# Optimization experiments

Hardware: AMD Instinct MI355X
Metric: run time of the kernel (lower is better)

## Reference

```python
import jax, jax.numpy as jnp
import numpy as np

N, E, D_IN, D_H = 20000, 320000, 512, 512
ALPHA = 0.1
LAMBDA = 1.0

def setup_inputs() -> dict:
    key = jax.random.key(0)
    ks = jax.random.split(key, 12)
    feat = jax.random.normal(ks[0], (N, D_IN), dtype=jnp.float32)
    src = jax.random.randint(ks[1], (E,), 0, N, dtype=jnp.int32)
    dst = jax.random.randint(ks[2], (E,), 0, N, dtype=jnp.int32)
    s = 0.05
    fc_w = jax.random.normal(ks[3], (D_H, D_IN), dtype=jnp.float32) * s  # torch Linear: [out,in]
    fc_b = jax.random.normal(ks[4], (D_H,), dtype=jnp.float32) * s
    w1_1 = jax.random.normal(ks[5], (D_H, D_H), dtype=jnp.float32) * s
    w2_1 = jax.random.normal(ks[6], (D_H, D_H), dtype=jnp.float32) * s
    b_1 = jax.random.normal(ks[7], (D_H,), dtype=jnp.float32) * s
    w1_2 = jax.random.normal(ks[8], (D_H, D_H), dtype=jnp.float32) * s
    w2_2 = jax.random.normal(ks[9], (D_H, D_H), dtype=jnp.float32) * s
    b_2 = jax.random.normal(ks[10], (D_H,), dtype=jnp.float32) * s
    return {"feat": feat, "src": src, "dst": dst, "fc_w": fc_w, "fc_b": fc_b,
            "w1_1": w1_1, "w2_1": w2_1, "b_1": b_1,
            "w1_2": w1_2, "w2_2": w2_2, "b_2": b_2}


def _gcn2_layer(h, h0, src, dst, norm, w1, w2, b, layer):
    # DGL GCN2Conv (project_initial_features=False)
    beta = float(np.log(LAMBDA / layer + 1.0))
    x = h * norm                      # [N, D]
    agg = jax.ops.segment_sum(x[src], dst, num_segments=h.shape[0])  # SpMM: sum over in-neighbors
    agg = agg * norm
    f = agg * (1.0 - ALPHA)
    f0 = h0 * ALPHA
    rst = ((1.0 - beta) * f + beta * (f @ w1)
           + (1.0 - beta) * f0 + beta * (f0 @ w2) + b)
    return jax.nn.relu(rst)


def reference(feat, src, dst, fc_w, fc_b, w1_1, w2_1, b_1, w1_2, w2_2, b_2):
    n = feat.shape[0]
    h = feat @ fc_w.T + fc_b          # initial projection
    # symmetric norm from in-degrees (clamped at 1), as in DGL
    deg = jax.ops.segment_sum(jnp.ones_like(dst, dtype=h.dtype), dst, num_segments=n)
    norm = jnp.clip(deg, 1.0, None) ** -0.5
    norm = norm[:, None]
    res = _gcn2_layer(h, h, src, dst, norm, w1_1, w2_1, b_1, layer=1)
    out = _gcn2_layer(res, h, src, dst, norm, w1_2, w2_2, b_2, layer=2)
    return out
```

## Files before the change

### kernel.cpp

```cpp
#include <hip/hip_runtime.h>
#include <hip/hip_bf16.h>
#include <stdint.h>
#include <stddef.h>

typedef __bf16 bf16_t;
typedef __bf16 bf16x4 __attribute__((ext_vector_type(4)));
typedef __bf16 bf16x8 __attribute__((ext_vector_type(8)));
typedef float floatx4 __attribute__((ext_vector_type(4)));

#define NN 20000
#define EE 320000
#define DD 512
#define CAP 96
#define BETA1 0.6931471805599453f
#define BETA2 0.40546510810816444f

__device__ __forceinline__ void gload16(const bf16_t* g, bf16_t* l) {
  __builtin_amdgcn_global_load_lds((const __attribute__((address_space(1))) uint32_t*)g,
                                   (__attribute__((address_space(3))) uint32_t*)l, 16, 0, 0);
}

__global__ __launch_bounds__(256) void bucket_kernel(
    const int* __restrict__ src, const int* __restrict__ dst,
    int* __restrict__ cnt, int* __restrict__ esrc, int E) {
  int e = blockIdx.x * 256 + threadIdx.x;
  if (e < E) {
    int d = dst[e];
    int pos = atomicAdd(&cnt[d], 1);
    if (pos < CAP) esrc[d * CAP + pos] = src[e];
  }
}

#define PREP_BLOCKS 7594
__global__ __launch_bounds__(256) void prep_kernel(
    const float* __restrict__ feat, const float* __restrict__ fc_w,
    const float* __restrict__ w1_1, const float* __restrict__ w2_1,
    const float* __restrict__ w1_2, const float* __restrict__ w2_2,
    bf16_t* __restrict__ featb, bf16_t* __restrict__ bw0,
    bf16_t* __restrict__ bt1, bf16_t* __restrict__ bt2,
    int* __restrict__ cnt, int* __restrict__ esrc) {
  int b = blockIdx.x, t = threadIdx.x;
  if (b < 5128) {
    const float* in = (b < 5000) ? feat : fc_w;
    bf16_t* out = (b < 5000) ? featb : bw0;
    size_t c = (size_t)(b < 5000 ? b : b - 5000) * 256 + t;
    const float* s = in + c * 8;
    float4 v0 = *(const float4*)s, v1 = *(const float4*)(s + 4);
    bf16x8 o = {(bf16_t)v0.x, (bf16_t)v0.y, (bf16_t)v0.z, (bf16_t)v0.w,
                (bf16_t)v1.x, (bf16_t)v1.y, (bf16_t)v1.z, (bf16_t)v1.w};
    *(bf16x8*)(out + c * 8) = o;
  } else if (b < 5640) {
    int base = (b < 5384) ? 5128 : 5384;
    const float* Wa = (b < 5384) ? w1_1 : w1_2;
    const float* Wb = (b < 5384) ? w2_1 : w2_2;
    bf16_t* bt = (b < 5384) ? bt1 : bt2;
    int c = (b - base) * 256 + t;
    int n = c >> 7, kc = c & 127;
    const float* W = (kc < 64) ? Wa : Wb;
    const float sc = (kc < 64) ? 1.0f : 0.1f;
    int kcw = kc & 63;
    bf16x8 o;
#pragma unroll
    for (int e = 0; e < 8; ++e)
      o[e] = (bf16_t)(sc * W[(size_t)(kcw * 8 + e) * 512 + n]);
    *(bf16x8*)(bt + (size_t)n * 1024 + kc * 8) = o;
  } else if (b < 5719) {
    int i = (b - 5640) * 256 + t;
    if (i < NN) cnt[i] = 0;
  } else {
    int i = (b - 5719) * 256 + t;
    ((int4*)esrc)[i] = make_int4(0, 0, 0, 0);
  }
}

__global__ __launch_bounds__(256) void aggregate_kernel(
    const bf16_t* __restrict__ hs, const int* __restrict__ cnt,
    const int* __restrict__ esrc, bf16_t* __restrict__ Acat) {
  __shared__ bf16_t ring[4][2][4][512];
  const int w = threadIdx.x >> 6;
  const int lane = threadIdx.x & 63;
  const int node = blockIdx.x * 4 + w;
  const int* eb = esrc + (size_t)node * CAP;
  int ncnt = cnt[node];
  int n_e = ncnt < CAP ? ncnt : CAP;
  float nd = 0.9f * rsqrtf(fmaxf((float)ncnt, 1.0f));
  int nchunks = (n_e + 3) >> 2;

  float acc[8] = {};
  bf16_t* r0base = &ring[w][0][0][lane * 8];
  bf16_t* r1base = &ring[w][1][0][lane * 8];

  int4 icur, inext;

  asm volatile("s_waitcnt vmcnt(0)" ::: "memory");
  __builtin_amdgcn_sched_barrier(0);
  icur = *(const int4*)(eb);
  asm volatile("s_waitcnt vmcnt(0)" ::: "memory");
  __builtin_amdgcn_sched_barrier(0);
  inext = *(const int4*)(eb + 4);
  gload16(hs + (size_t)icur.x * DD + lane * 8, r0base);
  gload16(hs + (size_t)icur.y * DD + lane * 8, r0base + 512);
  gload16(hs + (size_t)icur.z * DD + lane * 8, r0base + 1024);
  gload16(hs + (size_t)icur.w * DD + lane * 8, r0base + 1536);

  for (int c = 0; c < nchunks; ++c) {
    asm volatile("s_waitcnt vmcnt(4)" ::: "memory");
    __builtin_amdgcn_sched_barrier(0);
    int4 iuse = inext;
    int off2 = (c + 2) * 4; off2 = off2 > CAP - 4 ? CAP - 4 : off2;
    inext = *(const int4*)(eb + off2);
    bf16_t* rbn = ((c + 1) & 1) ? r1base : r0base;
    gload16(hs + (size_t)iuse.x * DD + lane * 8, rbn);
    gload16(hs + (size_t)iuse.y * DD + lane * 8, rbn + 512);
    gload16(hs + (size_t)iuse.z * DD + lane * 8, rbn + 1024);
    gload16(hs + (size_t)iuse.w * DD + lane * 8, rbn + 1536);
    asm volatile("s_waitcnt vmcnt(5)" ::: "memory");
    __builtin_amdgcn_sched_barrier(0);
    bf16_t* rb = (c & 1) ? r1base : r0base;
    bf16x8 v0 = *(const bf16x8*)(rb);
    bf16x8 v1 = *(const bf16x8*)(rb + 512);
    bf16x8 v2 = *(const bf16x8*)(rb + 1024);
    bf16x8 v3 = *(const bf16x8*)(rb + 1536);
    int e0 = c * 4;
    if (e0 < n_e) {
#pragma unroll
      for (int k = 0; k < 8; ++k) acc[k] += (float)v0[k];
    }
    if (e0 + 1 < n_e) {
#pragma unroll
      for (int k = 0; k < 8; ++k) acc[k] += (float)v1[k];
    }
    if (e0 + 2 < n_e) {
#pragma unroll
      for (int k = 0; k < 8; ++k) acc[k] += (float)v2[k];
    }
    if (e0 + 3 < n_e) {
#pragma unroll
      for (int k = 0; k < 8; ++k) acc[k] += (float)v3[k];
    }
  }

  bf16x8 ob;
#pragma unroll
  for (int k = 0; k < 8; ++k) ob[k] = (bf16_t)(nd * acc[k]);
  *(bf16x8*)(Acat + (size_t)node * 1024 + lane * 8) = ob;
}

template <int MODE>
__global__ __launch_bounds__(256) void gemm_kernel(
    const bf16_t* __restrict__ A, const bf16_t* __restrict__ BT,
    int lda, int ldb, int K, int M,
    const float* __restrict__ bias,
    const bf16_t* __restrict__ acat_ro, float beta,
    float* __restrict__ outf, bf16_t* __restrict__ outb,
    bf16_t* __restrict__ acat2,
    const int* __restrict__ cnt) {
  __shared__ bf16_t As[2][64 * 64];
  __shared__ bf16_t Bs[2][128 * 64];

  const int bid = blockIdx.x;
  const int mt = (bid >> 5) * 8 + (bid & 7);
  const int nt = (bid >> 3) & 3;
  const int m0 = mt * 64;
  if (m0 >= M) return;
  const int n0 = nt * 128;

  const int t = threadIdx.x;
  const int lane = t & 63;
  const int w = t >> 6;
  const int wm = w & 1, wn = w >> 1;
  const int quad = lane >> 4, m16 = lane & 15;

  const int tr = t >> 3;
  const int gc = (t & 7) ^ (tr & 7);
  int arow0 = m0 + tr;      arow0 = arow0 < M ? arow0 : M - 1;
  int arow1 = m0 + tr + 32; arow1 = arow1 < M ? arow1 : M - 1;
  const bf16_t* agp0 = A + (size_t)arow0 * lda + gc * 8;
  const bf16_t* agp1 = A + (size_t)arow1 * lda + gc * 8;
  const bf16_t* bgp0 = BT + (size_t)(n0 + tr) * ldb + gc * 8;
  const bf16_t* bgp1 = BT + (size_t)(n0 + tr + 32) * ldb + gc * 8;
  const bf16_t* bgp2 = BT + (size_t)(n0 + tr + 64) * ldb + gc * 8;
  const bf16_t* bgp3 = BT + (size_t)(n0 + tr + 96) * ldb + gc * 8;

#define STAGE(buf, ko)                              \
  gload16(agp0 + (ko), &As[buf][t * 8]);            \
  gload16(agp1 + (ko), &As[buf][(t + 256) * 8]);    \
  gload16(bgp0 + (ko), &Bs[buf][t * 8]);            \
  gload16(bgp1 + (ko), &Bs[buf][(t + 256) * 8]);    \
  gload16(bgp2 + (ko), &Bs[buf][(t + 512) * 8]);    \
  gload16(bgp3 + (ko), &Bs[buf][(t + 768) * 8]);

  floatx4 acc[2][4] = {};
  const int niter = K >> 6;

  STAGE(0, 0)

  for (int kt = 0; kt < niter; ++kt) {
    __syncthreads();
    const int b = kt & 1;
    if (kt + 1 < niter) {
      const int ko = (kt + 1) * 64;
      STAGE(b ^ 1, ko)
    }

#pragma unroll
    for (int ks = 0; ks < 2; ++ks) {
      bf16x8 af[2], bfr[4];
#pragma unroll
      for (int i = 0; i < 2; ++i) {
        int arow = wm * 32 + i * 16 + m16;
        int cc = (ks * 4 + quad) ^ (arow & 7);
        af[i] = *(const bf16x8*)(&As[b][(arow * 8 + cc) * 8]);
      }
#pragma unroll
      for (int j = 0; j < 4; ++j) {
        int brow = wn * 64 + j * 16 + m16;
        int cc = (ks * 4 + quad) ^ (brow & 7);
        bfr[j] = *(const bf16x8*)(&Bs[b][(brow * 8 + cc) * 8]);
      }
#pragma unroll
      for (int i = 0; i < 2; ++i)
#pragma unroll
        for (int j = 0; j < 4; ++j)
          acc[i][j] = __builtin_amdgcn_mfma_f32_16x16x32_bf16(af[i], bfr[j], acc[i][j], 0, 0, 0);
    }
  }
#undef STAGE

  float rsv[2][4];
  if constexpr (MODE != 2) {
#pragma unroll
    for (int i = 0; i < 2; ++i)
#pragma unroll
      for (int p = 0; p < 4; ++p) {
        int row = m0 + wm * 32 + i * 16 + quad * 4 + p;
        int rowc = row < M ? row : M - 1;
        rsv[i][p] = rsqrtf(fmaxf((float)cnt[rowc], 1.0f));
      }
  }

#pragma unroll
  for (int i = 0; i < 2; ++i) {
#pragma unroll
    for (int j = 0; j < 4; ++j) {
      int col = n0 + wn * 64 + j * 16 + m16;
      float bv = bias[col];
#pragma unroll
      for (int p = 0; p < 4; ++p) {
        int row = m0 + wm * 32 + i * 16 + quad * 4 + p;
        if (row < M) {
          float v = acc[i][j][p];
          if constexpr (MODE == 0) {
            float hv = v + bv;
            acat2[(size_t)row * 1024 + 512 + col] = (bf16_t)hv;
            outb[(size_t)row * DD + col] = (bf16_t)(rsv[i][p] * hv);
          } else {
            size_t idx = (size_t)row * DD + col;
            float fsv = (float)acat_ro[(size_t)row * 1024 + col] +
                        0.1f * (float)acat_ro[(size_t)row * 1024 + 512 + col];
            float r = (1.0f - beta) * fsv + beta * v + bv;
            r = fmaxf(r, 0.0f);
            if constexpr (MODE == 1) outb[idx] = (bf16_t)(rsv[i][p] * r);
            else outf[idx] = r;
          }
        }
      }
    }
  }
}

extern "C" void kernel_launch(void* const* d_in, const int* in_sizes, int n_in,
                              void* d_out, int out_size, void* d_ws, size_t ws_size,
                              hipStream_t stream) {
  const float* feat = (const float*)d_in[0];
  const int* src = (const int*)d_in[1];
  const int* dst = (const int*)d_in[2];
  const float* fc_w = (const float*)d_in[3];
  const float* fc_b = (const float*)d_in[4];
  const float* w1_1 = (const float*)d_in[5];
  const float* w2_1 = (const float*)d_in[6];
  const float* b_1  = (const float*)d_in[7];
  const float* w1_2 = (const float*)d_in[8];
  const float* w2_2 = (const float*)d_in[9];
  const float* b_2  = (const float*)d_in[10];
  float* out = (float*)d_out;

  char* ws = (char*)d_ws;
  size_t off = 0;
  auto alloc = [&](size_t bytes) {
    char* p = ws + off;
    off += (bytes + 255) & ~(size_t)255;
    return p;
  };
  const size_t NDf = (size_t)NN * DD;
  bf16_t* res_bf = (bf16_t*)alloc(NDf * sizeof(bf16_t));
  bf16_t* featb  = (bf16_t*)alloc(NDf * sizeof(bf16_t));
  bf16_t* hs     = (bf16_t*)alloc(NDf * sizeof(bf16_t));
  bf16_t* Acat   = (bf16_t*)alloc((size_t)NN * 1024 * sizeof(bf16_t));
  bf16_t* BW0    = (bf16_t*)alloc((size_t)512 * 512 * sizeof(bf16_t));
  bf16_t* BT1    = (bf16_t*)alloc((size_t)512 * 1024 * sizeof(bf16_t));
  bf16_t* BT2    = (bf16_t*)alloc((size_t)512 * 1024 * sizeof(bf16_t));
  int*    cnt    = (int*)alloc((size_t)NN * sizeof(int));
  int*    esrc   = (int*)alloc(((size_t)NN * CAP + 64) * sizeof(int));

  prep_kernel<<<PREP_BLOCKS, 256, 0, stream>>>(feat, fc_w, w1_1, w2_1, w1_2, w2_2,
                                               featb, BW0, BT1, BT2, cnt, esrc);
  bucket_kernel<<<(EE + 255) / 256, 256, 0, stream>>>(src, dst, cnt, esrc, EE);

  gemm_kernel<0><<<1280, 256, 0, stream>>>(featb, BW0, 512, 512, 512, NN, fc_b,
                                           nullptr, 0.0f, nullptr, hs, Acat, cnt);

  aggregate_kernel<<<NN / 4, 256, 0, stream>>>(hs, cnt, esrc, Acat);
  gemm_kernel<1><<<1280, 256, 0, stream>>>(Acat, BT1, 1024, 1024, 1024, NN, b_1,
                                           Acat, BETA1, nullptr, res_bf, nullptr, cnt);

  aggregate_kernel<<<NN / 4, 256, 0, stream>>>(res_bf, cnt, esrc, Acat);
  gemm_kernel<2><<<1280, 256, 0, stream>>>(Acat, BT2, 1024, 1024, 1024, NN, b_2,
                                           Acat, BETA2, out, nullptr, nullptr, nullptr);
}
```

Before: 342.6 us.

## Triple-buffer neighbor gather ring and tile the weight transpose through LDS

The aggregation kernel's LDS ring grows from two to three chunk buffers. Two chunks of neighbor rows are now prefetched before the loop, and the mid-loop wait is removed, so more gather loads are in flight while the current chunk is summed. Separately, the weight transpose-and-convert in the prep kernel now goes through a 32x32 shared-memory tile, so its global reads and writes are coalesced instead of strided. The larger ring raises LDS per block, which could lower occupancy in the aggregation kernel.

```diff
diff --git a/kernel.cpp b/kernel.cpp
--- a/kernel.cpp
+++ b/kernel.cpp
@@ -31,7 +31,7 @@
   }
 }
 
-#define PREP_BLOCKS 7594
+#define PREP_BLOCKS 8106
 __global__ __launch_bounds__(256) void prep_kernel(
     const float* __restrict__ feat, const float* __restrict__ fc_w,
     const float* __restrict__ w1_1, const float* __restrict__ w2_1,
@@ -39,6 +39,7 @@
     bf16_t* __restrict__ featb, bf16_t* __restrict__ bw0,
     bf16_t* __restrict__ bt1, bf16_t* __restrict__ bt2,
     int* __restrict__ cnt, int* __restrict__ esrc) {
+  __shared__ bf16_t tile[32][33];
   int b = blockIdx.x, t = threadIdx.x;
   if (b < 5128) {
     const float* in = (b < 5000) ? feat : fc_w;
@@ -49,26 +50,30 @@
     bf16x8 o = {(bf16_t)v0.x, (bf16_t)v0.y, (bf16_t)v0.z, (bf16_t)v0.w,
                 (bf16_t)v1.x, (bf16_t)v1.y, (bf16_t)v1.z, (bf16_t)v1.w};
     *(bf16x8*)(out + c * 8) = o;
-  } else if (b < 5640) {
-    int base = (b < 5384) ? 5128 : 5384;
-    const float* Wa = (b < 5384) ? w1_1 : w1_2;
-    const float* Wb = (b < 5384) ? w2_1 : w2_2;
-    bf16_t* bt = (b < 5384) ? bt1 : bt2;
-    int c = (b - base) * 256 + t;
-    int n = c >> 7, kc = c & 127;
-    const float* W = (kc < 64) ? Wa : Wb;
-    const float sc = (kc < 64) ? 1.0f : 0.1f;
-    int kcw = kc & 63;
-    bf16x8 o;
-#pragma unroll
-    for (int e = 0; e < 8; ++e)
-      o[e] = (bf16_t)(sc * W[(size_t)(kcw * 8 + e) * 512 + n]);
-    *(bf16x8*)(bt + (size_t)n * 1024 + kc * 8) = o;
-  } else if (b < 5719) {
-    int i = (b - 5640) * 256 + t;
+  } else if (b < 6152) {
+    int base = (b < 5640) ? 5128 : 5640;
+    const float* Wa = (b < 5640) ? w1_1 : w1_2;
+    const float* Wb = (b < 5640) ? w2_1 : w2_2;
+    bf16_t* bt = (b < 5640) ? bt1 : bt2;
+    int bb = b - base;
+    int n0 = (bb & 15) * 32;
+    int k0 = (bb >> 4) * 32;
+    int tx = t & 31, ty = t >> 5;
+    const float* W = (k0 < 512) ? Wa : Wb;
+    float sc = (k0 < 512) ? 1.0f : 0.1f;
+    int kk = k0 & 511;
+#pragma unroll
+    for (int i = 0; i < 32; i += 8)
+      tile[ty + i][tx] = (bf16_t)(sc * W[(size_t)(kk + ty + i) * 512 + n0 + tx]);
+    __syncthreads();
+#pragma unroll
+    for (int i = 0; i < 32; i += 8)
+      bt[(size_t)(n0 + ty + i) * 1024 + k0 + tx] = tile[tx][ty + i];
+  } else if (b < 6231) {
+    int i = (b - 6152) * 256 + t;
     if (i < NN) cnt[i] = 0;
   } else {
-    int i = (b - 5719) * 256 + t;
+    int i = (b - 6231) * 256 + t;
     ((int4*)esrc)[i] = make_int4(0, 0, 0, 0);
   }
 }
@@ -76,7 +81,7 @@
 __global__ __launch_bounds__(256) void aggregate_kernel(
     const bf16_t* __restrict__ hs, const int* __restrict__ cnt,
     const int* __restrict__ esrc, bf16_t* __restrict__ Acat) {
-  __shared__ bf16_t ring[4][2][4][512];
+  __shared__ bf16_t ring[4][3][4][512];
   const int w = threadIdx.x >> 6;
   const int lane = threadIdx.x & 63;
   const int node = blockIdx.x * 4 + w;
@@ -87,36 +92,40 @@
   int nchunks = (n_e + 3) >> 2;
 
   float acc[8] = {};
-  bf16_t* r0base = &ring[w][0][0][lane * 8];
-  bf16_t* r1base = &ring[w][1][0][lane * 8];
-
-  int4 icur, inext;
+  bf16_t* rb0 = &ring[w][0][0][lane * 8];
+  bf16_t* rb1 = &ring[w][1][0][lane * 8];
+  bf16_t* rb2 = &ring[w][2][0][lane * 8];
 
   asm volatile("s_waitcnt vmcnt(0)" ::: "memory");
   __builtin_amdgcn_sched_barrier(0);
-  icur = *(const int4*)(eb);
+  int4 i0 = *(const int4*)(eb);
   asm volatile("s_waitcnt vmcnt(0)" ::: "memory");
   __builtin_amdgcn_sched_barrier(0);
-  inext = *(const int4*)(eb + 4);
-  gload16(hs + (size_t)icur.x * DD + lane * 8, r0base);
-  gload16(hs + (size_t)icur.y * DD + lane * 8, r0base + 512);
-  gload16(hs + (size_t)icur.z * DD + lane * 8, r0base + 1024);
-  gload16(hs + (size_t)icur.w * DD + lane * 8, r0base + 1536);
+  int4 i1 = *(const int4*)(eb + 4);
+  asm volatile("s_waitcnt vmcnt(0)" ::: "memory");
+  __builtin_amdgcn_sched_barrier(0);
+  gload16(hs + (size_t)i0.x * DD + lane * 8, rb0);
+  gload16(hs + (size_t)i0.y * DD + lane * 8, rb0 + 512);
+  gload16(hs + (size_t)i0.z * DD + lane * 8, rb0 + 1024);
+  gload16(hs + (size_t)i0.w * DD + lane * 8, rb0 + 1536);
+  int4 inext = *(const int4*)(eb + 8);
+  gload16(hs + (size_t)i1.x * DD + lane * 8, rb1);
+  gload16(hs + (size_t)i1.y * DD + lane * 8, rb1 + 512);
+  gload16(hs + (size_t)i1.z * DD + lane * 8, rb1 + 1024);
+  gload16(hs + (size_t)i1.w * DD + lane * 8, rb1 + 1536);
 
   for (int c = 0; c < nchunks; ++c) {
     asm volatile("s_waitcnt vmcnt(4)" ::: "memory");
     __builtin_amdgcn_sched_barrier(0);
     int4 iuse = inext;
-    int off2 = (c + 2) * 4; off2 = off2 > CAP - 4 ? CAP - 4 : off2;
-    inext = *(const int4*)(eb + off2);
-    bf16_t* rbn = ((c + 1) & 1) ? r1base : r0base;
+    int off = (c + 3) * 4; off = off > CAP - 4 ? CAP - 4 : off;
+    inext = *(const int4*)(eb + off);
+    bf16_t* rbn = (c % 3 == 0) ? rb2 : (c % 3 == 1) ? rb0 : rb1;
     gload16(hs + (size_t)iuse.x * DD + lane * 8, rbn);
     gload16(hs + (size_t)iuse.y * DD + lane * 8, rbn + 512);
     gload16(hs + (size_t)iuse.z * DD + lane * 8, rbn + 1024);
     gload16(hs + (size_t)iuse.w * DD + lane * 8, rbn + 1536);
-    asm volatile("s_waitcnt vmcnt(5)" ::: "memory");
-    __builtin_amdgcn_sched_barrier(0);
-    bf16_t* rb = (c & 1) ? r1base : r0base;
+    bf16_t* rb = (c % 3 == 0) ? rb0 : (c % 3 == 1) ? rb1 : rb2;
     bf16x8 v0 = *(const bf16x8*)(rb);
     bf16x8 v1 = *(const bf16x8*)(rb + 512);
     bf16x8 v2 = *(const bf16x8*)(rb + 1024);
```

Result: slower. 349.7 us (+2.1%).
